# Kernel optimization log

Hardware: AMD Instinct MI355X
Metric: run time of the kernel (lower is better)

Reference implementation:

```python
import jax, jax.numpy as jnp
import numpy as np

EPS = 1e-8
INTRA_MARGIN_USED = 1.5  # combine() swaps margins: intra gets delta_dist
INTER_MARGIN_USED = 0.5  # inter gets delta_var
INTRA_W, INTER_W, REG_W = 1.0, 1.0, 0.001


def setup_inputs() -> dict:
    key = jax.random.key(0)
    k1, k2 = jax.random.split(key)
    N, D, K = 1000000, 32, 64
    features = jax.random.normal(k1, (N, D), dtype=jnp.float32)
    labels = jax.random.randint(k2, (N,), 0, K, dtype=jnp.int64 if jax.config.jax_enable_x64 else jnp.int32)
    return {"features": features, "labels": labels, "num_clusters": K}


def reference(features, labels, num_clusters):
    K = int(num_clusters)
    N, D = features.shape
    ones = jnp.ones((N,), dtype=features.dtype)
    counts = jax.ops.segment_sum(ones, labels, num_segments=K)            # (K,)
    sums = jax.ops.segment_sum(features, labels, num_segments=K)          # (K, D)
    safe_counts = jnp.maximum(counts, 1.0)
    means = sums / safe_counts[:, None]                                   # (K, D) cluster centroids

    # --- intra (variance) loss; margin = 1.5 due to original swap ---
    diff = features - means[labels] + EPS                                 # (N, D)
    dists = jnp.sqrt(jnp.sum(diff * diff, axis=1))                        # (N,)
    hinge2 = jnp.square(jnp.maximum(dists - INTRA_MARGIN_USED, 0.0))
    per_cluster = jax.ops.segment_sum(hinge2, labels, num_segments=K) / safe_counts
    intra_loss = jnp.mean(per_cluster)

    # --- inter (distance) loss; margin = 0.5 due to original swap ---
    pdiff = means[:, None, :] - means[None, :, :] + EPS                   # (K, K, D)
    pdist = jnp.sqrt(jnp.sum(pdiff * pdiff, axis=-1))                     # (K, K)
    hinge = jnp.square(jnp.maximum(2.0 * INTER_MARGIN_USED - pdist, 0.0))
    offdiag = 1.0 - jnp.eye(K, dtype=features.dtype)
    inter_loss = jnp.sum(hinge * offdiag) / float((K - 1) * K)

    # --- regularization ---
    reg_loss = jnp.mean(jnp.sqrt(jnp.sum(jnp.square(means + EPS), axis=1)))

    total = INTRA_W * intra_loss + INTER_W * inter_loss + REG_W * reg_loss
    return total
```

## Files before the change

kernel.cpp:

```cpp
#include <hip/hip_runtime.h>
#include <math.h>


#define EPS_F 1e-8f
constexpr int D = 32;
constexpr int K = 64;
constexpr int NPTS = 1024;
constexpr int P1 = K * D + K;
constexpr int NCH = 64;
constexpr int NBLK2 = 2048;

__global__ __launch_bounds__(256, 8) void pass1_kernel(
    const float* __restrict__ feat, const int* __restrict__ lab,
    float* __restrict__ part1, int N)
{
    __shared__ int            s_lab[NPTS];
    __shared__ unsigned short s_idx[NPTS];
    __shared__ int            s_hist[K];
    __shared__ int            s_pref[K];
    __shared__ int            s_cur[K];

    const int tid = threadIdx.x;
    const long long base = (long long)blockIdx.x * NPTS;
    int npts = (int)((long long)N - base);
    if (npts > NPTS) npts = NPTS;

    if (tid < K) s_hist[tid] = 0;
    __syncthreads();

    const int n4 = npts >> 2;
    for (int i4 = tid; i4 < n4; i4 += 256) {
        const int4 v = ((const int4*)(lab + base))[i4];
        s_lab[i4 * 4 + 0] = v.x; s_lab[i4 * 4 + 1] = v.y;
        s_lab[i4 * 4 + 2] = v.z; s_lab[i4 * 4 + 3] = v.w;
        atomicAdd(&s_hist[v.x], 1); atomicAdd(&s_hist[v.y], 1);
        atomicAdd(&s_hist[v.z], 1); atomicAdd(&s_hist[v.w], 1);
    }
    for (int i = (n4 << 2) + tid; i < npts; i += 256) {
        const int l = lab[base + i];
        s_lab[i] = l;
        atomicAdd(&s_hist[l], 1);
    }
    __syncthreads();

    if (tid < 64) {
        const int h = s_hist[tid];
        int v = h;
        for (int off = 1; off < 64; off <<= 1) {
            const int up = __shfl_up(v, off);
            if (tid >= off) v += up;
        }
        s_pref[tid] = v - h;
        s_cur[tid]  = v - h;
    }
    __syncthreads();

    for (int i = tid; i < npts; i += 256) {
        const int l = s_lab[i];
        const int pos = atomicAdd(&s_cur[l], 1);
        s_idx[pos] = (unsigned short)i;
    }
    __syncthreads();

    const int k = tid >> 2, q = tid & 3;
    const int start = s_pref[k], len = s_hist[k];
    float4 a0 = {0.f, 0.f, 0.f, 0.f}, a1 = {0.f, 0.f, 0.f, 0.f};
    int i = 0;
    for (; i + 2 <= len; i += 2) {
        const int i0 = s_idx[start + i];
        const int i1 = s_idx[start + i + 1];
        const float4* r0 = (const float4*)(feat + (base + i0) * D + q * 8);
        const float4* r1 = (const float4*)(feat + (base + i1) * D + q * 8);
        const float4 x0 = r0[0], y0 = r0[1];
        const float4 x1 = r1[0], y1 = r1[1];
        a0.x += x0.x + x1.x; a0.y += x0.y + x1.y;
        a0.z += x0.z + x1.z; a0.w += x0.w + x1.w;
        a1.x += y0.x + y1.x; a1.y += y0.y + y1.y;
        a1.z += y0.z + y1.z; a1.w += y0.w + y1.w;
    }
    if (i < len) {
        const int i0 = s_idx[start + i];
        const float4* r0 = (const float4*)(feat + (base + i0) * D + q * 8);
        const float4 x0 = r0[0], y0 = r0[1];
        a0.x += x0.x; a0.y += x0.y; a0.z += x0.z; a0.w += x0.w;
        a1.x += y0.x; a1.y += y0.y; a1.z += y0.z; a1.w += y0.w;
    }
    float* outp = part1 + (long long)blockIdx.x * P1;
    ((float4*)outp)[tid * 2 + 0] = a0;
    ((float4*)outp)[tid * 2 + 1] = a1;
    if (tid < K) outp[K * D + tid] = (float)s_hist[tid];
}

__global__ __launch_bounds__(256) void reduce1_kernel(
    const float* __restrict__ part1, float* __restrict__ part2,
    int chsz, int nblk1)
{
    const int e = blockIdx.x * 256 + threadIdx.x;
    if (e >= P1) return;
    const int y = blockIdx.y;
    const int b0 = y * chsz;
    int b1 = b0 + chsz; if (b1 > nblk1) b1 = nblk1;
    float s = 0.f;
    for (int b = b0; b < b1; b++) s += part1[(long long)b * P1 + e];
    part2[(long long)y * P1 + e] = s;
}

__global__ __launch_bounds__(256) void mean_kernel(
    const float* __restrict__ part2,
    float* __restrict__ means, float* __restrict__ icnt)
{
    const int e = blockIdx.x * blockDim.x + threadIdx.x;
    if (e >= P1) return;
    if (e < K * D) {
        float s = 0.f, c = 0.f;
        const int k = e >> 5;
        for (int y = 0; y < NCH; y++) {
            s += part2[(long long)y * P1 + e];
            c += part2[(long long)y * P1 + K * D + k];
        }
        means[e] = s / fmaxf(c, 1.0f);
    } else {
        float s = 0.f;
        for (int y = 0; y < NCH; y++) s += part2[(long long)y * P1 + e];
        icnt[e - K * D] = 1.0f / fmaxf(s, 1.0f);
    }
}

__global__ __launch_bounds__(256, 8) void pass2_kernel(
    const float* __restrict__ feat, const int* __restrict__ lab,
    const float* __restrict__ means, const float* __restrict__ icnt,
    float* __restrict__ hpart, int N)
{
    __shared__ float s_red[256];
    const int tid  = threadIdx.x;
    const int sub  = tid & 7;
    const int pofs = tid >> 3;
    const long long stride = (long long)NBLK2 * 32;
    float racc = 0.f;
    for (long long p = (long long)blockIdx.x * 32 + pofs; p < N; p += stride) {
        const int l = lab[p];
        const float4 f = *(const float4*)(feat + p * D + sub * 4);
        const float4 m = *(const float4*)(means + l * D + sub * 4);
        const float dx = f.x - m.x + EPS_F;
        const float dy = f.y - m.y + EPS_F;
        const float dz = f.z - m.z + EPS_F;
        const float dw = f.w - m.w + EPS_F;
        float acc = dx * dx + dy * dy + dz * dz + dw * dw;
        acc += __shfl_xor(acc, 1);
        acc += __shfl_xor(acc, 2);
        acc += __shfl_xor(acc, 4);
        if (sub == 0) {
            const float dist = sqrtf(acc);
            const float h = fmaxf(dist - 1.5f, 0.f);
            racc += h * h * icnt[l];
        }
    }
    s_red[tid] = racc;
    __syncthreads();
    for (int st = 128; st; st >>= 1) { if (tid < st) s_red[tid] += s_red[tid + st]; __syncthreads(); }
    if (tid == 0) hpart[blockIdx.x] = s_red[0];
}

__global__ __launch_bounds__(256) void final_kernel(
    const float* __restrict__ hpart,
    const float* __restrict__ means, float* __restrict__ out)
{
    __shared__ float s_m[K * D];
    __shared__ float s_red[256];
    const int tid = threadIdx.x;
    for (int i = tid; i < K * D; i += 256) s_m[i] = means[i];

    float hs = 0.f;
    for (int b = tid; b < NBLK2; b += 256) hs += hpart[b];
    s_red[tid] = hs;
    __syncthreads();
    for (int s = 128; s; s >>= 1) { if (tid < s) s_red[tid] += s_red[tid + s]; __syncthreads(); }
    float total = 0.f;
    if (tid == 0) total = s_red[0] * (1.0f / K);
    __syncthreads();

    float mj[32];
    const int j = tid & 63;
    {
        const float4* mrow = (const float4*)(means + j * D);
        #pragma unroll
        for (int q = 0; q < 8; q++) {
            const float4 t = mrow[q];
            mj[q * 4 + 0] = t.x; mj[q * 4 + 1] = t.y;
            mj[q * 4 + 2] = t.z; mj[q * 4 + 3] = t.w;
        }
    }
    float isum = 0.f;
    const int igrp = tid >> 6;
    for (int ii = 0; ii < 16; ii++) {
        const int i = igrp * 16 + ii;
        const float4* srow = (const float4*)(s_m + i * D);
        float d2 = 0.f;
        #pragma unroll
        for (int q = 0; q < 8; q++) {
            const float4 mv = srow[q];
            const float a0 = mv.x - mj[q * 4 + 0] + EPS_F;
            const float a1 = mv.y - mj[q * 4 + 1] + EPS_F;
            const float a2 = mv.z - mj[q * 4 + 2] + EPS_F;
            const float a3 = mv.w - mj[q * 4 + 3] + EPS_F;
            d2 += a0 * a0 + a1 * a1 + a2 * a2 + a3 * a3;
        }
        if (i != j) {
            const float pd = sqrtf(d2);
            const float h = fmaxf(1.0f - pd, 0.f);
            isum += h * h;
        }
    }
    s_red[tid] = isum;
    __syncthreads();
    for (int s = 128; s; s >>= 1) { if (tid < s) s_red[tid] += s_red[tid + s]; __syncthreads(); }
    if (tid == 0) total += s_red[0] * (1.0f / ((K - 1) * K));
    __syncthreads();

    float r = 0.f;
    if (tid < 64) {
        float d2 = 0.f;
        #pragma unroll
        for (int d = 0; d < 32; d++) { const float t = mj[d] + EPS_F; d2 += t * t; }
        r = sqrtf(d2);
    }
    s_red[tid] = r;
    __syncthreads();
    for (int s = 128; s; s >>= 1) { if (tid < s) s_red[tid] += s_red[tid + s]; __syncthreads(); }
    if (tid == 0) out[0] = total + 0.001f * (s_red[0] * (1.0f / K));
}

extern "C" void kernel_launch(void* const* d_in, const int* in_sizes, int n_in,
                              void* d_out, int out_size, void* d_ws, size_t ws_size,
                              hipStream_t stream)
{
    const float* feat = (const float*)d_in[0];
    const int*   lab  = (const int*)d_in[1];
    const int N = in_sizes[1];

    float* ws = (float*)d_ws;

    const int nblk1 = (N + NPTS - 1) / NPTS;
    const int chsz  = (nblk1 + NCH - 1) / NCH;

    float* means = ws;
    float* icnt  = means + K * D;
    float* part2 = icnt + K;
    float* hpart = part2 + (long long)NCH * P1;
    float* part1 = hpart + NBLK2;

    pass1_kernel<<<nblk1, 256, 0, stream>>>(feat, lab, part1, N);
    reduce1_kernel<<<dim3((P1 + 255) / 256, NCH), 256, 0, stream>>>(part1, part2, chsz, nblk1);
    mean_kernel<<<(P1 + 255) / 256, 256, 0, stream>>>(part2, means, icnt);
    pass2_kernel<<<NBLK2, 256, 0, stream>>>(feat, lab, means, icnt, hpart, N);
    final_kernel<<<1, 256, 0, stream>>>(hpart, means, (float*)d_out);
}
```

Measured before the change: 69.50 us.

## Stage means in padded LDS, one-thread-per-point pass2, move inter/reg loss into pass2

Pass2 now loads the centroids and inverse counts into padded shared memory and has each thread process a whole point: it reads 8 float4 per row and computes the distance without cross-lane shuffles. This replaces the old 8-lanes-per-point layout, which gathered centroid rows from global memory and kept only one lane in eight busy on the hinge math. The pairwise inter-cluster and regularisation terms move into block 0 of pass2, which shrinks the final kernel to a plain sum. Pass1's gather loop is unrolled to four rows and both kernels' launch-bounds occupancy hint drops from 8 to 4. In exchange, per-thread row loads are strided 128 bytes apart, which may hurt coalescing, and block 0 carries extra serial work.

Result: faster. 65.76 us (-5.4%).

```diff
diff --git a/kernel.cpp b/kernel.cpp
--- a/kernel.cpp
+++ b/kernel.cpp
@@ -9,8 +9,9 @@
 constexpr int P1 = K * D + K;
 constexpr int NCH = 64;
 constexpr int NBLK2 = 2048;
-
-__global__ __launch_bounds__(256, 8) void pass1_kernel(
+constexpr int MPAD = 40;
+
+__global__ __launch_bounds__(256, 4) void pass1_kernel(
     const float* __restrict__ feat, const int* __restrict__ lab,
     float* __restrict__ part1, int N)
 {
@@ -66,19 +67,29 @@
     const int start = s_pref[k], len = s_hist[k];
     float4 a0 = {0.f, 0.f, 0.f, 0.f}, a1 = {0.f, 0.f, 0.f, 0.f};
     int i = 0;
-    for (; i + 2 <= len; i += 2) {
-        const int i0 = s_idx[start + i];
+    for (; i + 4 <= len; i += 4) {
+        const int i0 = s_idx[start + i + 0];
         const int i1 = s_idx[start + i + 1];
+        const int i2 = s_idx[start + i + 2];
+        const int i3 = s_idx[start + i + 3];
         const float4* r0 = (const float4*)(feat + (base + i0) * D + q * 8);
         const float4* r1 = (const float4*)(feat + (base + i1) * D + q * 8);
+        const float4* r2 = (const float4*)(feat + (base + i2) * D + q * 8);
+        const float4* r3 = (const float4*)(feat + (base + i3) * D + q * 8);
         const float4 x0 = r0[0], y0 = r0[1];
         const float4 x1 = r1[0], y1 = r1[1];
-        a0.x += x0.x + x1.x; a0.y += x0.y + x1.y;
-        a0.z += x0.z + x1.z; a0.w += x0.w + x1.w;
-        a1.x += y0.x + y1.x; a1.y += y0.y + y1.y;
-        a1.z += y0.z + y1.z; a1.w += y0.w + y1.w;
-    }
-    if (i < len) {
+        const float4 x2 = r2[0], y2 = r2[1];
+        const float4 x3 = r3[0], y3 = r3[1];
+        a0.x += (x0.x + x1.x) + (x2.x + x3.x);
+        a0.y += (x0.y + x1.y) + (x2.y + x3.y);
+        a0.z += (x0.z + x1.z) + (x2.z + x3.z);
+        a0.w += (x0.w + x1.w) + (x2.w + x3.w);
+        a1.x += (y0.x + y1.x) + (y2.x + y3.x);
+        a1.y += (y0.y + y1.y) + (y2.y + y3.y);
+        a1.z += (y0.z + y1.z) + (y2.z + y3.z);
+        a1.w += (y0.w + y1.w) + (y2.w + y3.w);
+    }
+    for (; i < len; ++i) {
         const int i0 = s_idx[start + i];
         const float4* r0 = (const float4*)(feat + (base + i0) * D + q * 8);
         const float4 x0 = r0[0], y0 = r0[1];
@@ -126,95 +137,78 @@
     }
 }
 
-__global__ __launch_bounds__(256, 8) void pass2_kernel(
+__global__ __launch_bounds__(256, 4) void pass2_kernel(
     const float* __restrict__ feat, const int* __restrict__ lab,
     const float* __restrict__ means, const float* __restrict__ icnt,
-    float* __restrict__ hpart, int N)
-{
-    __shared__ float s_red[256];
-    const int tid  = threadIdx.x;
-    const int sub  = tid & 7;
-    const int pofs = tid >> 3;
-    const long long stride = (long long)NBLK2 * 32;
-    float racc = 0.f;
-    for (long long p = (long long)blockIdx.x * 32 + pofs; p < N; p += stride) {
-        const int l = lab[p];
-        const float4 f = *(const float4*)(feat + p * D + sub * 4);
-        const float4 m = *(const float4*)(means + l * D + sub * 4);
-        const float dx = f.x - m.x + EPS_F;
-        const float dy = f.y - m.y + EPS_F;
-        const float dz = f.z - m.z + EPS_F;
-        const float dw = f.w - m.w + EPS_F;
-        float acc = dx * dx + dy * dy + dz * dz + dw * dw;
-        acc += __shfl_xor(acc, 1);
-        acc += __shfl_xor(acc, 2);
-        acc += __shfl_xor(acc, 4);
-        if (sub == 0) {
-            const float dist = sqrtf(acc);
-            const float h = fmaxf(dist - 1.5f, 0.f);
-            racc += h * h * icnt[l];
-        }
-    }
-    s_red[tid] = racc;
-    __syncthreads();
-    for (int st = 128; st; st >>= 1) { if (tid < st) s_red[tid] += s_red[tid + st]; __syncthreads(); }
-    if (tid == 0) hpart[blockIdx.x] = s_red[0];
-}
-
-__global__ __launch_bounds__(256) void final_kernel(
-    const float* __restrict__ hpart,
-    const float* __restrict__ means, float* __restrict__ out)
-{
-    __shared__ float s_m[K * D];
+    float* __restrict__ hpart, float* __restrict__ ir, int N)
+{
+    __shared__ float s_m[K * MPAD];
+    __shared__ float s_ic[K];
     __shared__ float s_red[256];
     const int tid = threadIdx.x;
-    for (int i = tid; i < K * D; i += 256) s_m[i] = means[i];
-
-    float hs = 0.f;
-    for (int b = tid; b < NBLK2; b += 256) hs += hpart[b];
-    s_red[tid] = hs;
-    __syncthreads();
-    for (int s = 128; s; s >>= 1) { if (tid < s) s_red[tid] += s_red[tid + s]; __syncthreads(); }
-    float total = 0.f;
-    if (tid == 0) total = s_red[0] * (1.0f / K);
-    __syncthreads();
-
+
+    for (int e = tid; e < K * D; e += 256)
+        s_m[(e >> 5) * MPAD + (e & 31)] = means[e];
+    if (tid < K) s_ic[tid] = icnt[tid];
+    __syncthreads();
+
+    float racc = 0.f;
+    const long long stride = (long long)NBLK2 * 256;
+    for (long long p = (long long)blockIdx.x * 256 + tid; p < N; p += stride) {
+        const int l = lab[p];
+        const float4* frow = (const float4*)(feat + p * D);
+        float4 fv[8];
+        #pragma unroll
+        for (int j = 0; j < 8; j++) fv[j] = frow[j];
+        const float* mrow = s_m + l * MPAD;
+        float d2 = 0.f;
+        #pragma unroll
+        for (int j = 0; j < 8; j++) {
+            const float4 mv = *(const float4*)(mrow + j * 4);
+            const float dx = fv[j].x - mv.x + EPS_F;
+            const float dy = fv[j].y - mv.y + EPS_F;
+            const float dz = fv[j].z - mv.z + EPS_F;
+            const float dw = fv[j].w - mv.w + EPS_F;
+            d2 += dx * dx + dy * dy + dz * dz + dw * dw;
+        }
+        const float h = fmaxf(sqrtf(d2) - 1.5f, 0.f);
+        racc += h * h * s_ic[l];
+    }
+    s_red[tid] = racc;
+    __syncthreads();
+    for (int st = 128; st; st >>= 1) { if (tid < st) s_red[tid] += s_red[tid + st]; __syncthreads(); }
+    if (tid == 0) hpart[blockIdx.x] = s_red[0];
+
+    if (blockIdx.x != 0) return;
+    __syncthreads();
     float mj[32];
     const int j = tid & 63;
-    {
-        const float4* mrow = (const float4*)(means + j * D);
-        #pragma unroll
-        for (int q = 0; q < 8; q++) {
-            const float4 t = mrow[q];
-            mj[q * 4 + 0] = t.x; mj[q * 4 + 1] = t.y;
-            mj[q * 4 + 2] = t.z; mj[q * 4 + 3] = t.w;
-        }
-    }
+    #pragma unroll
+    for (int d = 0; d < 32; d++) mj[d] = s_m[j * MPAD + d];
     float isum = 0.f;
     const int igrp = tid >> 6;
     for (int ii = 0; ii < 16; ii++) {
         const int i = igrp * 16 + ii;
-        const float4* srow = (const float4*)(s_m + i * D);
+        const float4* srow = (const float4*)(s_m + i * MPAD);
         float d2 = 0.f;
         #pragma unroll
         for (int q = 0; q < 8; q++) {
             const float4 mv = srow[q];
-            const float a0 = mv.x - mj[q * 4 + 0] + EPS_F;
-            const float a1 = mv.y - mj[q * 4 + 1] + EPS_F;
-            const float a2 = mv.z - mj[q * 4 + 2] + EPS_F;
-            const float a3 = mv.w - mj[q * 4 + 3] + EPS_F;
-            d2 += a0 * a0 + a1 * a1 + a2 * a2 + a3 * a3;
+            const float b0 = mv.x - mj[q * 4 + 0] + EPS_F;
+            const float b1 = mv.y - mj[q * 4 + 1] + EPS_F;
+            const float b2 = mv.z - mj[q * 4 + 2] + EPS_F;
+            const float b3 = mv.w - mj[q * 4 + 3] + EPS_F;
+            d2 += b0 * b0 + b1 * b1 + b2 * b2 + b3 * b3;
         }
         if (i != j) {
-            const float pd = sqrtf(d2);
-            const float h = fmaxf(1.0f - pd, 0.f);
+            const float h = fmaxf(1.0f - sqrtf(d2), 0.f);
             isum += h * h;
         }
     }
     s_red[tid] = isum;
     __syncthreads();
-    for (int s = 128; s; s >>= 1) { if (tid < s) s_red[tid] += s_red[tid + s]; __syncthreads(); }
-    if (tid == 0) total += s_red[0] * (1.0f / ((K - 1) * K));
+    for (int st = 128; st; st >>= 1) { if (tid < st) s_red[tid] += s_red[tid + st]; __syncthreads(); }
+    if (tid == 0) ir[0] = s_red[0] * (1.0f / ((K - 1) * K));
     __syncthreads();
 
     float r = 0.f;
@@ -226,8 +220,22 @@
     }
     s_red[tid] = r;
     __syncthreads();
-    for (int s = 128; s; s >>= 1) { if (tid < s) s_red[tid] += s_red[tid + s]; __syncthreads(); }
-    if (tid == 0) out[0] = total + 0.001f * (s_red[0] * (1.0f / K));
+    for (int st = 128; st; st >>= 1) { if (tid < st) s_red[tid] += s_red[tid + st]; __syncthreads(); }
+    if (tid == 0) ir[1] = s_red[0] * (1.0f / K);
+}
+
+__global__ __launch_bounds__(256) void final_kernel(
+    const float* __restrict__ hpart, const float* __restrict__ ir,
+    float* __restrict__ out)
+{
+    __shared__ float s_red[256];
+    const int tid = threadIdx.x;
+    float hs = 0.f;
+    for (int b = tid; b < NBLK2; b += 256) hs += hpart[b];
+    s_red[tid] = hs;
+    __syncthreads();
+    for (int st = 128; st; st >>= 1) { if (tid < st) s_red[tid] += s_red[tid + st]; __syncthreads(); }
+    if (tid == 0) out[0] = s_red[0] * (1.0f / K) + ir[0] + 0.001f * ir[1];
 }
 
 extern "C" void kernel_launch(void* const* d_in, const int* in_sizes, int n_in,
@@ -245,13 +253,14 @@
 
     float* means = ws;
     float* icnt  = means + K * D;
-    float* part2 = icnt + K;
+    float* ir    = icnt + K;
+    float* part2 = ir + 4;
     float* hpart = part2 + (long long)NCH * P1;
     float* part1 = hpart + NBLK2;
 
     pass1_kernel<<<nblk1, 256, 0, stream>>>(feat, lab, part1, N);
     reduce1_kernel<<<dim3((P1 + 255) / 256, NCH), 256, 0, stream>>>(part1, part2, chsz, nblk1);
     mean_kernel<<<(P1 + 255) / 256, 256, 0, stream>>>(part2, means, icnt);
-    pass2_kernel<<<NBLK2, 256, 0, stream>>>(feat, lab, means, icnt, hpart, N);
-    final_kernel<<<1, 256, 0, stream>>>(hpart, means, (float*)d_out);
-}
+    pass2_kernel<<<NBLK2, 256, 0, stream>>>(feat, lab, means, icnt, hpart, ir, N);
+    final_kernel<<<1, 256, 0, stream>>>(hpart, ir, (float*)d_out);
+}
```
